# Kernel tuning notes

Hardware: AMD Instinct MI355X
Metric: run time of the kernel (lower is better)

Reference implementation:

```python
import jax, jax.numpy as jnp
import numpy as np

S_NUM, E_NUM, K, B = 50000, 20000, 128, 8192
N = S_NUM + E_NUM
N_EDGES = 1000000
LAYERS = 3


def setup_inputs() -> dict:
    key = jax.random.key(0)
    ks = jax.random.split(key, 16)
    return {
        "stu_emb": jax.random.normal(ks[0], (S_NUM, K), jnp.float32),
        "exer_emb": jax.random.normal(ks[1], (E_NUM, K), jnp.float32),
        "kn_emb": jax.random.normal(ks[2], (K, K), jnp.float32),
        "disc_emb": jax.random.normal(ks[3], (E_NUM, 1), jnp.float32),
        "right_W": jax.random.normal(ks[4], (LAYERS, K, K), jnp.float32) * (1.0 / np.sqrt(K)),
        "wrong_W": jax.random.normal(ks[5], (LAYERS, K, K), jnp.float32) * (1.0 / np.sqrt(K)),
        "right_ci": jax.random.uniform(ks[6], (N, 1), jnp.float32),
        "right_cj": jax.random.uniform(ks[7], (N, 1), jnp.float32),
        "wrong_ci": jax.random.uniform(ks[8], (N, 1), jnp.float32),
        "wrong_cj": jax.random.uniform(ks[9], (N, 1), jnp.float32),
        "right_edges": jax.random.randint(ks[10], (2, N_EDGES), 0, N, jnp.int64),
        "wrong_edges": jax.random.randint(ks[11], (2, N_EDGES), 0, N, jnp.int64),
        "student_id": jax.random.randint(ks[12], (B,), 0, S_NUM, jnp.int64),
        "exercise_id": jax.random.randint(ks[13], (B,), 0, E_NUM, jnp.int64),
    }


def _gcmc_layer(feat, W, cj, ci, src, dst, n_nodes):
    # dense projection + src-side normalizer (dropout is identity in eval)
    h = (feat @ W) * cj                    # [N, K]
    # copy_u/sum message passing: scatter-add messages to destination nodes
    agg = jax.ops.segment_sum(h[src], dst, num_segments=n_nodes)  # [N, K]
    return agg * ci


def _graph_forward(feat, Ws, ci, cj, edges, n_nodes):
    src, dst = edges[0], edges[1]
    for i in range(Ws.shape[0]):
        feat = _gcmc_layer(feat, Ws[i], cj, ci, src, dst, n_nodes)
    return feat


def reference(stu_emb, exer_emb, kn_emb, disc_emb, right_W, wrong_W,
              right_ci, right_cj, wrong_ci, wrong_cj,
              right_edges, wrong_edges, student_id, exercise_id):
    n_students = stu_emb.shape[0]
    n_nodes = stu_emb.shape[0] + exer_emb.shape[0]
    all_weight = jnp.concatenate([stu_emb, exer_emb], axis=0)  # [N, K]
    w1 = _graph_forward(all_weight, right_W, right_ci, right_cj, right_edges, n_nodes)
    w2 = _graph_forward(all_weight, wrong_W, wrong_ci, wrong_cj, wrong_edges, n_nodes)
    stu_forward = w1[:n_students] + w2[:n_students]
    exer_forward = w1[n_students:] + w2[n_students:]
    batch_stu_ts = stu_forward[student_id]      # [B, K]
    batch_exer_ts = exer_forward[exercise_id]   # [B, K]
    disc_ts = disc_emb[exercise_id]             # [B, 1]
    knowledge_ts = kn_emb                       # [K, K]
    return (batch_stu_ts, batch_exer_ts, disc_ts, knowledge_ts)
```

## Files before the change

### kernel.cpp

```cpp
#include <hip/hip_runtime.h>
#include <hip/hip_bf16.h>
#include <stdint.h>

#define S_NUM 50000
#define E_NUM 20000
#define NNODE 70000
#define KDIM 128
#define BATCH 8192
#define NEDGE 1000000

#define NRANGE 128
#define RSZ 547
#define BUCKET_CAP 8448
#define RCAP 16672
#define CHUNK 8192
#define BINCAP 120
#define GR 256
#define CAPC 16384

typedef __attribute__((ext_vector_type(8))) short short8;
typedef __attribute__((ext_vector_type(4))) float f32x4;
typedef __attribute__((ext_vector_type(2))) float f32x2;

__device__ __forceinline__ float bf2f(ushort u) {
    union { uint32_t i; float f; } v; v.i = ((uint32_t)u) << 16; return v.f;
}
__device__ __forceinline__ ushort f2bf(float f) {
    union { uint32_t i; float f; } v; v.f = f;
    uint32_t r = v.i + 0x7fffu + ((v.i >> 16) & 1u);
    return (ushort)(r >> 16);
}
__device__ __forceinline__ f32x2 up2(uint32_t u) {
    union { uint32_t i; float f; } lo, hi;
    lo.i = u << 16; hi.i = u & 0xffff0000u;
    f32x2 r; r.x = lo.f; r.y = hi.f; return r;
}

__global__ void prepW_k(const float* __restrict__ rW, const float* __restrict__ wW,
                        ushort* __restrict__ ws, int* __restrict__ gbcnt,
                        int* __restrict__ flags, int* __restrict__ nsel) {
    int t = blockIdx.x * blockDim.x + threadIdx.x;
    if (blockIdx.x == 0 && threadIdx.x < 256) gbcnt[threadIdx.x] = 0;
    if (t == 0) nsel[0] = 0;
    if (t < NNODE) flags[t] = 0;
    if (t >= 6 * 16384) return;
    int m = t >> 14, idx = t & 16383;
    const float* W = (m < 3) ? rW + m * 16384 : wW + (m - 3) * 16384;
    float x = W[idx];
    int k = idx >> 7, c = idx & 127;
    ushort hb = f2bf(x);
    ushort lb = f2bf(x - bf2f(hb));
    int off = ((c * 256 + 2 * k) ^ ((c & 7) << 4)) >> 1;
    ws[(size_t)m * 32768 + off] = hb;
    ws[(size_t)m * 32768 + 16384 + off] = lb;
}

__global__ __launch_bounds__(256) void bucket_k(const int* __restrict__ redge,
                                                const int* __restrict__ wedge,
                                                int* __restrict__ gbcnt,
                                                uint32_t* __restrict__ bpk) {
    __shared__ uint32_t lpk[NRANGE][BINCAP];
    __shared__ int lcnt[NRANGE];
    __shared__ int gbase[NRANGE];
    const int NB = (NEDGE + CHUNK - 1) / CHUNK;
    int bid = blockIdx.x;
    int graph = bid >= NB;
    int cb = graph ? bid - NB : bid;
    const int* eg = graph ? wedge : redge;
    int e0 = cb * CHUNK;
    int nthis = min(CHUNK, NEDGE - e0);
    for (int i = threadIdx.x; i < NRANGE; i += 256) lcnt[i] = 0;
    __syncthreads();
    for (int i = threadIdx.x; i < nthis; i += 256) {
        int s = eg[e0 + i];
        int d = eg[NEDGE + e0 + i];
        int b = d / RSZ;
        uint32_t p = ((uint32_t)(d - b * RSZ) << 17) | (uint32_t)s;
        int slot = atomicAdd(&lcnt[b], 1);
        if (slot < BINCAP) lpk[b][slot] = p;
        else {
            int gs = atomicAdd(&gbcnt[graph * NRANGE + b], 1);
            if (gs < BUCKET_CAP)
                bpk[(size_t)(graph * NRANGE + b) * BUCKET_CAP + gs] = p;
        }
    }
    __syncthreads();
    for (int b = threadIdx.x; b < NRANGE; b += 256) {
        int c = min(lcnt[b], BINCAP);
        lcnt[b] = c;
        gbase[b] = atomicAdd(&gbcnt[graph * NRANGE + b], c);
    }
    __syncthreads();
    for (int b = 0; b < NRANGE; ++b) {
        int c = lcnt[b];
        size_t base = (size_t)(graph * NRANGE + b) * BUCKET_CAP + gbase[b];
        for (int i = threadIdx.x; i < c; i += 256)
            if (gbase[b] + i < BUCKET_CAP) bpk[base + i] = lpk[b][i];
    }
}

__global__ __launch_bounds__(256) void build_k(const uint32_t* __restrict__ bpk,
                                               const int* __restrict__ gbcnt,
                                               int* __restrict__ rpb,
                                               int* __restrict__ rpe,
                                               int* __restrict__ csr) {
    __shared__ int lcnt[RSZ];
    __shared__ int lexcl[RSZ];
    __shared__ int pexcl[RSZ];
    __shared__ int lcur[RSZ];
    __shared__ int sliceB[BUCKET_CAP];
    __shared__ int wsum[4];
    __shared__ int s_carry;
    int combo = blockIdx.x;
    int graph = combo >> 7, grp = combo & (NRANGE - 1);
    int lo = grp * RSZ;
    int rsize = min(RSZ, NNODE - lo);
    int n = min(gbcnt[combo], BUCKET_CAP);
    const uint32_t* bp = bpk + (size_t)combo * BUCKET_CAP;
    int* rpbg = rpb + graph * NNODE;
    int* rpeg = rpe + graph * NNODE;
    int* og = csr + (size_t)combo * RCAP;
    const int rbase = combo * RCAP;
    int tid = threadIdx.x, lane = tid & 63, wid = tid >> 6;

    for (int i = tid; i < rsize; i += 256) lcnt[i] = 0;
    if (tid == 0) s_carry = 0;
    __syncthreads();
    for (int i = tid; i < n; i += 256)
        atomicAdd(&lcnt[bp[i] >> 17], 1);
    __syncthreads();
    for (int base = 0; base < rsize; base += 256) {
        int i = base + tid;
        int v = (i < rsize) ? lcnt[i] : 0;
        int incl = v;
        #pragma unroll
        for (int off = 1; off < 64; off <<= 1) {
            int t = __shfl_up(incl, off, 64);
            if (lane >= off) incl += t;
        }
        if (lane == 63) wsum[wid] = incl;
        __syncthreads();
        int carry = s_carry;
        if (wid == 0 && lane < 4) {
            int wv = wsum[lane];
            #pragma unroll
            for (int off = 1; off < 4; off <<= 1) {
                int t = __shfl_up(wv, off, 64);
                if (lane >= off) wv += t;
            }
            wsum[lane] = wv;
        }
        __syncthreads();
        int waveoff = (wid == 0) ? 0 : wsum[wid - 1];
        int excl = carry + waveoff + incl - v;
        if (i < rsize) { lexcl[i] = excl; lcur[i] = excl; }
        __syncthreads();
        if (tid == 0) s_carry = carry + wsum[3];
        __syncthreads();
    }
    if (tid == 0) s_carry = 0;
    __syncthreads();
    for (int base = 0; base < rsize; base += 256) {
        int i = base + tid;
        int v = (i < rsize) ? ((lcnt[i] + 15) & ~15) : 0;
        int incl = v;
        #pragma unroll
        for (int off = 1; off < 64; off <<= 1) {
            int t = __shfl_up(incl, off, 64);
            if (lane >= off) incl += t;
        }
        if (lane == 63) wsum[wid] = incl;
        __syncthreads();
        int carry = s_carry;
        if (wid == 0 && lane < 4) {
            int wv = wsum[lane];
            #pragma unroll
            for (int off = 1; off < 4; off <<= 1) {
                int t = __shfl_up(wv, off, 64);
                if (lane >= off) wv += t;
            }
            wsum[lane] = wv;
        }
        __syncthreads();
        int waveoff = (wid == 0) ? 0 : wsum[wid - 1];
        int excl = carry + waveoff + incl - v;
        if (i < rsize) pexcl[i] = excl;
        __syncthreads();
        if (tid == 0) s_carry = carry + wsum[3];
        __syncthreads();
    }
    for (int i = tid; i < rsize; i += 256) {
        int pc = (lcnt[i] + 15) & ~15;
        rpbg[lo + i] = rbase + pexcl[i];
        rpeg[lo + i] = rbase + pexcl[i] + pc;
    }
    for (int i = tid; i < n; i += 256) {
        uint32_t p = bp[i];
        int slot = atomicAdd(&lcur[p >> 17], 1);
        sliceB[slot] = (int)p;
    }
    __syncthreads();
    for (int i = tid; i < n; i += 256) {
        uint32_t p = (uint32_t)sliceB[i];
        int r = p >> 17;
        og[pexcl[r] + (i - lexcl[r])] = (int)(p & 0x1FFFFu);
    }
    for (int r = tid; r < rsize; r += 256) {
        int c = lcnt[r], pc = (c + 15) & ~15, b = pexcl[r];
        for (int j = c; j < pc; ++j) og[b + j] = NNODE;
    }
}

__global__ void mark_k(const int* __restrict__ sid, const int* __restrict__ eid,
                       int* __restrict__ flags) {
    int i = blockIdx.x * blockDim.x + threadIdx.x;
    if (i < BATCH) flags[sid[i]] = 1;
    else if (i < 2 * BATCH) flags[S_NUM + eid[i - BATCH]] = 1;
}

__global__ void compact_k(const int* __restrict__ flags, int* __restrict__ list,
                          int* __restrict__ inv, int* __restrict__ nsel) {
    for (int i = blockIdx.x * blockDim.x + threadIdx.x; i < NNODE;
         i += gridDim.x * blockDim.x) {
        if (flags[i]) {
            int pos = atomicAdd(nsel, 1);
            list[pos] = i;
            inv[i] = pos;
        }
    }
}

__global__ __launch_bounds__(256) void cvt1_k(const float* __restrict__ stu,
                                              const float* __restrict__ exer,
                                              const float* __restrict__ rcj,
                                              const float* __restrict__ wcj,
                                              uint4* __restrict__ featb,
                                              uint4* __restrict__ fcR,
                                              uint4* __restrict__ fcW,
                                              float* __restrict__ cjpR,
                                              float* __restrict__ cjpW) {
    const int main = NNODE * 16;
    const int total = main + 48 + 2 * (NNODE + 1);
    const uint4 z4 = {0, 0, 0, 0};
    for (int i = blockIdx.x * blockDim.x + threadIdx.x; i < total;
         i += gridDim.x * blockDim.x) {
        if (i < main) {
            int node = i >> 4;
            int qq = i & 15;
            const float4* src = (const float4*)((node < S_NUM)
                                  ? stu + (size_t)node * KDIM
                                  : exer + (size_t)(node - S_NUM) * KDIM);
            float4 a = src[qq * 2];
            float4 b = src[qq * 2 + 1];
            uint4 o;
            o.x = (uint32_t)f2bf(a.x) | ((uint32_t)f2bf(a.y) << 16);
            o.y = (uint32_t)f2bf(a.z) | ((uint32_t)f2bf(a.w) << 16);
            o.z = (uint32_t)f2bf(b.x) | ((uint32_t)f2bf(b.y) << 16);
            o.w = (uint32_t)f2bf(b.z) | ((uint32_t)f2bf(b.w) << 16);
            featb[i] = o;
        } else if (i < main + 48) {
            int j = i - main;
            size_t off = (size_t)NNODE * 16 + (j & 15);
            switch (j >> 4) {
                case 0: featb[off] = z4; break;
                case 1: fcR[off] = z4; break;
                default: fcW[off] = z4; break;
            }
        } else {
            int k = i - main - 48;
            if (k <= NNODE)  cjpR[k] = (k < NNODE) ? rcj[k] : 0.f;
            else {
                int m = k - (NNODE + 1);
                cjpW[m] = (m < NNODE) ? wcj[m] : 0.f;
            }
        }
    }
}

template<int USECJ, int COMPACT>
__global__ __launch_bounds__(256) void agg2_k(const uint4* __restrict__ srcR,
                                              const uint4* __restrict__ srcW,
                                              const float* __restrict__ cjR,
                                              const float* __restrict__ cjW,
                                              const int* __restrict__ rpb,
                                              const int* __restrict__ rpe,
                                              const int* __restrict__ csr,
                                              const int* __restrict__ list,
                                              const int* __restrict__ nselp,
                                              uint4* __restrict__ outR,
                                              uint4* __restrict__ outW) {
    int lane = threadIdx.x & 63, wid = threadIdx.x >> 6;
    int grp = lane >> 4, c16 = lane & 15;
    int gi = blockIdx.x * 16 + wid * 4 + grp;
    int graph, n, orow;
    if (COMPACT) {
        int nsel = nselp[0];
        graph = gi >= CAPC;
        int ci = graph ? gi - CAPC : gi;
        if (ci >= nsel) return;
        n = list[ci];
        orow = ci;
    } else {
        if (gi >= 2 * NNODE) return;
        graph = gi >= NNODE;
        n = graph ? gi - NNODE : gi;
        orow = n;
    }
    const uint4* fc = graph ? srcW : srcR;
    const float* cjg = graph ? cjW : cjR;
    int beg = (rpb + graph * NNODE)[n];
    int end = (rpe + graph * NNODE)[n];
    uint4* outp = graph ? outW : outR;

    f32x2 a0 = {0.f, 0.f}, a1 = {0.f, 0.f}, a2 = {0.f, 0.f}, a3 = {0.f, 0.f};
    for (int e = beg; e < end; e += 8) {
        int s0 = csr[e],     s1 = csr[e + 1], s2 = csr[e + 2], s3 = csr[e + 3];
        int s4 = csr[e + 4], s5 = csr[e + 5], s6 = csr[e + 6], s7 = csr[e + 7];
        uint4 u0 = fc[(size_t)s0 * 16 + c16];
        uint4 u1 = fc[(size_t)s1 * 16 + c16];
        uint4 u2 = fc[(size_t)s2 * 16 + c16];
        uint4 u3 = fc[(size_t)s3 * 16 + c16];
        uint4 u4 = fc[(size_t)s4 * 16 + c16];
        uint4 u5 = fc[(size_t)s5 * 16 + c16];
        uint4 u6 = fc[(size_t)s6 * 16 + c16];
        uint4 u7 = fc[(size_t)s7 * 16 + c16];
        if (USECJ) {
            float c0 = cjg[s0], c1 = cjg[s1], c2 = cjg[s2], c3 = cjg[s3];
            float c4 = cjg[s4], c5 = cjg[s5], c6 = cjg[s6], c7 = cjg[s7];
            f32x2 v0 = {c0, c0}, v1 = {c1, c1}, v2 = {c2, c2}, v3 = {c3, c3};
            f32x2 v4 = {c4, c4}, v5 = {c5, c5}, v6 = {c6, c6}, v7 = {c7, c7};
            a0 += v0 * up2(u0.x) + v1 * up2(u1.x) + v2 * up2(u2.x) + v3 * up2(u3.x)
                + v4 * up2(u4.x) + v5 * up2(u5.x) + v6 * up2(u6.x) + v7 * up2(u7.x);
            a1 += v0 * up2(u0.y) + v1 * up2(u1.y) + v2 * up2(u2.y) + v3 * up2(u3.y)
                + v4 * up2(u4.y) + v5 * up2(u5.y) + v6 * up2(u6.y) + v7 * up2(u7.y);
            a2 += v0 * up2(u0.z) + v1 * up2(u1.z) + v2 * up2(u2.z) + v3 * up2(u3.z)
                + v4 * up2(u4.z) + v5 * up2(u5.z) + v6 * up2(u6.z) + v7 * up2(u7.z);
            a3 += v0 * up2(u0.w) + v1 * up2(u1.w) + v2 * up2(u2.w) + v3 * up2(u3.w)
                + v4 * up2(u4.w) + v5 * up2(u5.w) + v6 * up2(u6.w) + v7 * up2(u7.w);
        } else {
            a0 += (up2(u0.x) + up2(u1.x)) + (up2(u2.x) + up2(u3.x))
                + (up2(u4.x) + up2(u5.x)) + (up2(u6.x) + up2(u7.x));
            a1 += (up2(u0.y) + up2(u1.y)) + (up2(u2.y) + up2(u3.y))
                + (up2(u4.y) + up2(u5.y)) + (up2(u6.y) + up2(u7.y));
            a2 += (up2(u0.z) + up2(u1.z)) + (up2(u2.z) + up2(u3.z))
                + (up2(u4.z) + up2(u5.z)) + (up2(u6.z) + up2(u7.z));
            a3 += (up2(u0.w) + up2(u1.w)) + (up2(u2.w) + up2(u3.w))
                + (up2(u4.w) + up2(u5.w)) + (up2(u6.w) + up2(u7.w));
        }
    }
    uint4 o;
    o.x = (uint32_t)f2bf(a0.x) | ((uint32_t)f2bf(a0.y) << 16);
    o.y = (uint32_t)f2bf(a1.x) | ((uint32_t)f2bf(a1.y) << 16);
    o.z = (uint32_t)f2bf(a2.x) | ((uint32_t)f2bf(a2.y) << 16);
    o.w = (uint32_t)f2bf(a3.x) | ((uint32_t)f2bf(a3.y) << 16);
    outp[(size_t)orow * 16 + c16] = o;
}

template<int COMPACT>
__global__ __launch_bounds__(256) void gemm2_k(const ushort* __restrict__ AR,
                                               const ushort* __restrict__ AW,
                                               const ushort* __restrict__ wsR,
                                               const ushort* __restrict__ wsW,
                                               const float* __restrict__ rci,
                                               const float* __restrict__ rcj,
                                               const float* __restrict__ wci,
                                               const float* __restrict__ wcj,
                                               const int* __restrict__ list,
                                               const int* __restrict__ nselp,
                                               ushort* __restrict__ outR,
                                               ushort* __restrict__ outW,
                                               int mode) {
    const int halfBlocks = COMPACT ? (CAPC / GR) : ((NNODE + GR - 1) / GR);
    int graph = blockIdx.x >= halfBlocks;
    int bb = graph ? blockIdx.x - halfBlocks : blockIdx.x;
    int nrows = COMPACT ? nselp[0] : NNODE;
    const ushort* A = graph ? AW : AR;
    const ushort* wsm = graph ? wsW : wsR;
    const float* ci = graph ? wci : rci;
    const float* cj = graph ? wcj : rcj;
    ushort* outB = graph ? outW : outR;

    __shared__ ushort wt[32768];
    {
        const uint4* g = (const uint4*)wsm;
        uint4* l = (uint4*)wt;
        for (int i = threadIdx.x; i < 4096; i += 256) l[i] = g[i];
    }
    __syncthreads();

    int wid = threadIdx.x >> 6, lane = threadIdx.x & 63;
    int q = lane >> 4, l16 = lane & 15;
    int rbase = bb * GR + wid * 64;
    if (rbase >= nrows) return;

    short8 z8 = {0, 0, 0, 0, 0, 0, 0, 0};
    short8 afr[4][4];
    #pragma unroll
    for (int t = 0; t < 4; ++t) {
        int row = rbase + t * 16 + l16;
        bool rok = row < nrows;
        const short8* ar = (const short8*)(A + (size_t)row * KDIM);
        #pragma unroll
        for (int kb = 0; kb < 4; ++kb)
            afr[t][kb] = rok ? ar[kb * 4 + q] : z8;
    }
    float scal[4][4];
    #pragma unroll
    for (int t = 0; t < 4; ++t)
        #pragma unroll
        for (int b = 0; b < 4; ++b) {
            int r = rbase + t * 16 + q * 4 + b;
            bool ok = r < nrows;
            int node = COMPACT ? (ok ? list[r] : 0) : r;
            scal[t][b] = ok ? (mode ? ci[node] * cj[node] : ci[node]) : 0.f;
        }

    #pragma unroll
    for (int cb = 0; cb < 8; ++cb) {
        int c = cb * 16 + l16;
        short8 bHi[4], bLo[4];
        #pragma unroll
        for (int kb = 0; kb < 4; ++kb) {
            int byte = (c * 256 + 2 * (kb * 32 + q * 8)) ^ ((c & 7) << 4);
            bHi[kb] = *(const short8*)((const char*)wt + byte);
            bLo[kb] = *(const short8*)((const char*)wt + 32768 + byte);
        }
        #pragma unroll
        for (int t = 0; t < 4; ++t) {
            f32x4 acc = {0.f, 0.f, 0.f, 0.f};
            #pragma unroll
            for (int kb = 0; kb < 4; ++kb) {
                acc = __builtin_amdgcn_mfma_f32_16x16x32_bf16(afr[t][kb], bHi[kb], acc, 0, 0, 0);
                acc = __builtin_amdgcn_mfma_f32_16x16x32_bf16(afr[t][kb], bLo[kb], acc, 0, 0, 0);
            }
            #pragma unroll
            for (int b = 0; b < 4; ++b) {
                int r = rbase + t * 16 + q * 4 + b;
                if (r < nrows)
                    outB[(size_t)r * KDIM + c] = f2bf(acc[b] * scal[t][b]);
            }
        }
    }
}

__global__ void out_k(const ushort* __restrict__ w1c, const ushort* __restrict__ w2c,
                      const int* __restrict__ inv,
                      const float* __restrict__ disc, const float* __restrict__ kn,
                      const int* __restrict__ sid, const int* __restrict__ eid,
                      float* __restrict__ out) {
    const int total = 2 * BATCH * KDIM + BATCH + KDIM * KDIM;
    for (int i = blockIdx.x * blockDim.x + threadIdx.x; i < total;
         i += gridDim.x * blockDim.x) {
        if (i < BATCH * KDIM) {
            int b = i >> 7, c = i & 127;
            size_t r = (size_t)inv[sid[b]];
            out[i] = bf2f(w1c[r * KDIM + c]) + bf2f(w2c[r * KDIM + c]);
        } else if (i < 2 * BATCH * KDIM) {
            int j = i - BATCH * KDIM;
            int b = j >> 7, c = j & 127;
            size_t r = (size_t)inv[S_NUM + eid[b]];
            out[i] = bf2f(w1c[r * KDIM + c]) + bf2f(w2c[r * KDIM + c]);
        } else if (i < 2 * BATCH * KDIM + BATCH) {
            out[i] = disc[eid[i - 2 * BATCH * KDIM]];
        } else {
            out[i] = kn[i - (2 * BATCH * KDIM + BATCH)];
        }
    }
}

static inline size_t align_up(size_t x) { return (x + 255) & ~(size_t)255; }

extern "C" void kernel_launch(void* const* d_in, const int* in_sizes, int n_in,
                              void* d_out, int out_size, void* d_ws, size_t ws_size,
                              hipStream_t stream) {
    const float* stu  = (const float*)d_in[0];
    const float* exer = (const float*)d_in[1];
    const float* kn   = (const float*)d_in[2];
    const float* disc = (const float*)d_in[3];
    const float* rW   = (const float*)d_in[4];
    const float* wW   = (const float*)d_in[5];
    const float* rci  = (const float*)d_in[6];
    const float* rcj  = (const float*)d_in[7];
    const float* wci  = (const float*)d_in[8];
    const float* wcj  = (const float*)d_in[9];
    const int* redge   = (const int*)d_in[10];
    const int* wedge   = (const int*)d_in[11];
    const int* sid     = (const int*)d_in[12];
    const int* eid     = (const int*)d_in[13];
    float* out         = (float*)d_out;

    char* p = (char*)d_ws;
    const size_t fB16 = align_up((size_t)(NNODE + 1) * KDIM * 2);
    ushort* featb = (ushort*)p; p += fB16;
    ushort* fcR = (ushort*)p; p += fB16;
    ushort* fcW = (ushort*)p; p += fB16;
    ushort* pR  = (ushort*)p; p += fB16;
    ushort* pW  = (ushort*)p; p += fB16;
    ushort* ws  = (ushort*)p; p += align_up((size_t)6 * 32768 * 2);
    int* gbcnt = (int*)p; p += align_up((size_t)256 * 4);
    int* rpb = (int*)p; p += align_up((size_t)2 * NNODE * 4);
    int* rpe = (int*)p; p += align_up((size_t)2 * NNODE * 4);
    int* csr = (int*)p; p += align_up((size_t)256 * RCAP * 4);
    float* cjpR = (float*)p; p += align_up((size_t)(NNODE + 1) * 4);
    float* cjpW = (float*)p; p += align_up((size_t)(NNODE + 1) * 4);
    int* flags = (int*)p; p += align_up((size_t)NNODE * 4);
    int* list  = (int*)p; p += align_up((size_t)CAPC * 4);
    int* inv   = (int*)p; p += align_up((size_t)NNODE * 4);
    int* nsel  = (int*)p; p += align_up((size_t)16 * 4);
    uint32_t* bpk = (uint32_t*)pR;
    ushort* w1c = featb;
    ushort* w2c = featb + (size_t)CAPC * KDIM;

    const int aggFull = (2 * NNODE + 15) / 16;
    const int aggComp = 2 * CAPC / 16;
    const int gemmFull = 2 * ((NNODE + GR - 1) / GR);
    const int gemmComp = 2 * (CAPC / GR);
    const int NB = (NEDGE + CHUNK - 1) / CHUNK;

    prepW_k<<<(6 * 16384 + 255) / 256, 256, 0, stream>>>(rW, wW, ws, gbcnt, flags, nsel);
    bucket_k<<<2 * NB, 256, 0, stream>>>(redge, wedge, gbcnt, bpk);
    build_k<<<256, 256, 0, stream>>>(bpk, gbcnt, rpb, rpe, csr);
    mark_k<<<(2 * BATCH + 255) / 256, 256, 0, stream>>>(sid, eid, flags);
    compact_k<<<(NNODE + 255) / 256, 256, 0, stream>>>(flags, list, inv, nsel);
    cvt1_k<<<2048, 256, 0, stream>>>(stu, exer, rcj, wcj, (uint4*)featb,
                                     (uint4*)fcR, (uint4*)fcW, cjpR, cjpW);

    agg2_k<1, 0><<<aggFull, 256, 0, stream>>>((const uint4*)featb, (const uint4*)featb,
                                              cjpR, cjpW, rpb, rpe, csr, nullptr, nullptr,
                                              (uint4*)pR, (uint4*)pW);
    gemm2_k<0><<<gemmFull, 256, 0, stream>>>(pR, pW, ws + 0 * 32768, ws + 3 * 32768,
                                             rci, rcj, wci, wcj, nullptr, nullptr,
                                             fcR, fcW, 1);
    agg2_k<0, 0><<<aggFull, 256, 0, stream>>>((const uint4*)fcR, (const uint4*)fcW,
                                              nullptr, nullptr, rpb, rpe, csr,
                                              nullptr, nullptr, (uint4*)pR, (uint4*)pW);
    gemm2_k<0><<<gemmFull, 256, 0, stream>>>(pR, pW, ws + 1 * 32768, ws + 4 * 32768,
                                             rci, rcj, wci, wcj, nullptr, nullptr,
                                             fcR, fcW, 1);
    agg2_k<0, 1><<<aggComp, 256, 0, stream>>>((const uint4*)fcR, (const uint4*)fcW,
                                              nullptr, nullptr, rpb, rpe, csr,
                                              list, nsel, (uint4*)pR, (uint4*)pW);
    gemm2_k<1><<<gemmComp, 256, 0, stream>>>(pR, pW, ws + 2 * 32768, ws + 5 * 32768,
                                             rci, rcj, wci, wcj, list, nsel,
                                             w1c, w2c, 0);

    out_k<<<2048, 256, 0, stream>>>(w1c, w2c, inv, disc, kn, sid, eid, out);
}
```

Measured before the change: 349.7 us.

## Split node features into four 32-column planes for cache-friendly gather aggregation

Stores bf16 node features as four column planes of 32 elements each, so every plane is about 4.5MB and fits in cache. The aggregation kernel now gives each block one plane and one graph, with 4 lanes per node reading 64 contiguous bytes, instead of 16 lanes reading a full 256-byte row. The GEMM input and output indexing and the conversion kernel are updated to match, and CSR indices are loaded as int4. The intent is to raise L2/MALL hit rates on random gathers, at the cost of reading the CSR index lists four times and doing narrower per-node work.

```diff
diff --git a/kernel.cpp b/kernel.cpp
--- a/kernel.cpp
+++ b/kernel.cpp
@@ -17,6 +17,7 @@
 #define BINCAP 120
 #define GR 256
 #define CAPC 16384
+#define NT 4
 
 typedef __attribute__((ext_vector_type(8))) short short8;
 typedef __attribute__((ext_vector_type(4))) float f32x4;
@@ -35,6 +36,12 @@
     lo.i = u << 16; hi.i = u & 0xffff0000u;
     f32x2 r; r.x = lo.f; r.y = hi.f; return r;
 }
+__device__ __forceinline__ uint32_t pk2(f32x2 a) {
+    return (uint32_t)f2bf(a.x) | ((uint32_t)f2bf(a.y) << 16);
+}
+
+#define PLANE_E ((size_t)(NNODE + 1) * 32)
+#define PLANE_U4 ((size_t)(NNODE + 1) * 4)
 
 __global__ void prepW_k(const float* __restrict__ rW, const float* __restrict__ wW,
                         ushort* __restrict__ ws, int* __restrict__ gbcnt,
@@ -257,15 +264,15 @@
             o.y = (uint32_t)f2bf(a.z) | ((uint32_t)f2bf(a.w) << 16);
             o.z = (uint32_t)f2bf(b.x) | ((uint32_t)f2bf(b.y) << 16);
             o.w = (uint32_t)f2bf(b.z) | ((uint32_t)f2bf(b.w) << 16);
-            featb[i] = o;
+            featb[(size_t)(qq >> 2) * PLANE_U4 + (size_t)node * 4 + (qq & 3)] = o;
         } else if (i < main + 48) {
             int j = i - main;
-            size_t off = (size_t)NNODE * 16 + (j & 15);
-            switch (j >> 4) {
-                case 0: featb[off] = z4; break;
-                case 1: fcR[off] = z4; break;
-                default: fcW[off] = z4; break;
-            }
+            int arr = j >> 4;
+            int jj = j & 15;
+            size_t off = (size_t)(jj >> 2) * PLANE_U4 + (size_t)NNODE * 4 + (jj & 3);
+            if (arr == 0)      featb[off] = z4;
+            else if (arr == 1) fcR[off] = z4;
+            else               fcW[off] = z4;
         } else {
             int k = i - main - 48;
             if (k <= NNODE)  cjpR[k] = (k < NNODE) ? rcj[k] : 0.f;
@@ -289,44 +296,40 @@
                                               const int* __restrict__ nselp,
                                               uint4* __restrict__ outR,
                                               uint4* __restrict__ outW) {
-    int lane = threadIdx.x & 63, wid = threadIdx.x >> 6;
-    int grp = lane >> 4, c16 = lane & 15;
-    int gi = blockIdx.x * 16 + wid * 4 + grp;
-    int graph, n, orow;
+    int combo = blockIdx.x & 7;
+    int tile = combo & 3, graph = combo >> 2;
+    int ci = (blockIdx.x >> 3) * 64 + (threadIdx.x >> 2);
+    int l4 = threadIdx.x & 3;
+    int n, orow;
     if (COMPACT) {
-        int nsel = nselp[0];
-        graph = gi >= CAPC;
-        int ci = graph ? gi - CAPC : gi;
-        if (ci >= nsel) return;
-        n = list[ci];
-        orow = ci;
+        if (ci >= nselp[0]) return;
+        n = list[ci]; orow = ci;
     } else {
-        if (gi >= 2 * NNODE) return;
-        graph = gi >= NNODE;
-        n = graph ? gi - NNODE : gi;
-        orow = n;
-    }
-    const uint4* fc = graph ? srcW : srcR;
+        if (ci >= NNODE) return;
+        n = ci; orow = ci;
+    }
+    const uint4* fc = (graph ? srcW : srcR) + (size_t)tile * PLANE_U4;
     const float* cjg = graph ? cjW : cjR;
     int beg = (rpb + graph * NNODE)[n];
     int end = (rpe + graph * NNODE)[n];
-    uint4* outp = graph ? outW : outR;
-
+    uint4* outp = (graph ? outW : outR) + (size_t)tile * PLANE_U4;
+
+    const int4* csr4 = (const int4*)csr;
     f32x2 a0 = {0.f, 0.f}, a1 = {0.f, 0.f}, a2 = {0.f, 0.f}, a3 = {0.f, 0.f};
     for (int e = beg; e < end; e += 8) {
-        int s0 = csr[e],     s1 = csr[e + 1], s2 = csr[e + 2], s3 = csr[e + 3];
-        int s4 = csr[e + 4], s5 = csr[e + 5], s6 = csr[e + 6], s7 = csr[e + 7];
-        uint4 u0 = fc[(size_t)s0 * 16 + c16];
-        uint4 u1 = fc[(size_t)s1 * 16 + c16];
-        uint4 u2 = fc[(size_t)s2 * 16 + c16];
-        uint4 u3 = fc[(size_t)s3 * 16 + c16];
-        uint4 u4 = fc[(size_t)s4 * 16 + c16];
-        uint4 u5 = fc[(size_t)s5 * 16 + c16];
-        uint4 u6 = fc[(size_t)s6 * 16 + c16];
-        uint4 u7 = fc[(size_t)s7 * 16 + c16];
+        int4 sa = csr4[e >> 2];
+        int4 sb = csr4[(e >> 2) + 1];
+        uint4 u0 = fc[(size_t)sa.x * 4 + l4];
+        uint4 u1 = fc[(size_t)sa.y * 4 + l4];
+        uint4 u2 = fc[(size_t)sa.z * 4 + l4];
+        uint4 u3 = fc[(size_t)sa.w * 4 + l4];
+        uint4 u4 = fc[(size_t)sb.x * 4 + l4];
+        uint4 u5 = fc[(size_t)sb.y * 4 + l4];
+        uint4 u6 = fc[(size_t)sb.z * 4 + l4];
+        uint4 u7 = fc[(size_t)sb.w * 4 + l4];
         if (USECJ) {
-            float c0 = cjg[s0], c1 = cjg[s1], c2 = cjg[s2], c3 = cjg[s3];
-            float c4 = cjg[s4], c5 = cjg[s5], c6 = cjg[s6], c7 = cjg[s7];
+            float c0 = cjg[sa.x], c1 = cjg[sa.y], c2 = cjg[sa.z], c3 = cjg[sa.w];
+            float c4 = cjg[sb.x], c5 = cjg[sb.y], c6 = cjg[sb.z], c7 = cjg[sb.w];
             f32x2 v0 = {c0, c0}, v1 = {c1, c1}, v2 = {c2, c2}, v3 = {c3, c3};
             f32x2 v4 = {c4, c4}, v5 = {c5, c5}, v6 = {c6, c6}, v7 = {c7, c7};
             a0 += v0 * up2(u0.x) + v1 * up2(u1.x) + v2 * up2(u2.x) + v3 * up2(u3.x)
@@ -349,11 +352,8 @@
         }
     }
     uint4 o;
-    o.x = (uint32_t)f2bf(a0.x) | ((uint32_t)f2bf(a0.y) << 16);
-    o.y = (uint32_t)f2bf(a1.x) | ((uint32_t)f2bf(a1.y) << 16);
-    o.z = (uint32_t)f2bf(a2.x) | ((uint32_t)f2bf(a2.y) << 16);
-    o.w = (uint32_t)f2bf(a3.x) | ((uint32_t)f2bf(a3.y) << 16);
-    outp[(size_t)orow * 16 + c16] = o;
+    o.x = pk2(a0); o.y = pk2(a1); o.z = pk2(a2); o.w = pk2(a3);
+    outp[(size_t)orow * 4 + l4] = o;
 }
 
 template<int COMPACT>
@@ -399,10 +399,11 @@
     for (int t = 0; t < 4; ++t) {
         int row = rbase + t * 16 + l16;
         bool rok = row < nrows;
-        const short8* ar = (const short8*)(A + (size_t)row * KDIM);
         #pragma unroll
         for (int kb = 0; kb < 4; ++kb)
-            afr[t][kb] = rok ? ar[kb * 4 + q] : z8;
+            afr[t][kb] = rok ? *(const short8*)(A + (size_t)kb * PLANE_E
+                                                + (size_t)row * 32 + q * 8)
+                             : z8;
     }
     float scal[4][4];
     #pragma unroll
@@ -436,8 +437,11 @@
             #pragma unroll
             for (int b = 0; b < 4; ++b) {
                 int r = rbase + t * 16 + q * 4 + b;
-                if (r < nrows)
-                    outB[(size_t)r * KDIM + c] = f2bf(acc[b] * scal[t][b]);
+                if (r < nrows) {
+                    ushort v = f2bf(acc[b] * scal[t][b]);
+                    if (COMPACT) outB[(size_t)r * KDIM + c] = v;
+                    else outB[(size_t)(c >> 5) * PLANE_E + (size_t)r * 32 + (c & 31)] = v;
+                }
             }
         }
     }
@@ -490,7 +494,7 @@
     float* out         = (float*)d_out;
 
     char* p = (char*)d_ws;
-    const size_t fB16 = align_up((size_t)(NNODE + 1) * KDIM * 2);
+    const size_t fB16 = align_up((size_t)NT * PLANE_E * 2);
     ushort* featb = (ushort*)p; p += fB16;
     ushort* fcR = (ushort*)p; p += fB16;
     ushort* fcW = (ushort*)p; p += fB16;
@@ -511,8 +515,8 @@
     ushort* w1c = featb;
     ushort* w2c = featb + (size_t)CAPC * KDIM;
 
-    const int aggFull = (2 * NNODE + 15) / 16;
-    const int aggComp = 2 * CAPC / 16;
+    const int aggFull = 8 * ((NNODE + 63) / 64);
+    const int aggComp = 8 * (CAPC / 64);
     const int gemmFull = 2 * ((NNODE + GR - 1) / GR);
     const int gemmComp = 2 * (CAPC / GR);
     const int NB = (NEDGE + CHUNK - 1) / CHUNK;
```

After: 374.2 us. +7.0%, slower.

## Fold three layer weight matrices into one product and defer GEMM to selected rows

Applied to the files above, without the earlier changes.

Since each layer is linear and the per-node scalings commute with the right multiplication by W, the three per-layer GEMMs are replaced by one precomputed product W1·W2·W3 per graph. It is applied only to the compacted rows needed for the output. Aggregation passes now carry per-source weights (cj, then ci*cj) instead of running intermediate full-size GEMMs. This removes two full-node GEMM passes at the cost of a small weight-product prelude. Intermediate features are kept in unprojected bf16 form, which changes rounding behaviour.

```diff
diff --git a/kernel.cpp b/kernel.cpp
--- a/kernel.cpp
+++ b/kernel.cpp
@@ -35,24 +35,66 @@
     lo.i = u << 16; hi.i = u & 0xffff0000u;
     f32x2 r; r.x = lo.f; r.y = hi.f; return r;
 }
-
-__global__ void prepW_k(const float* __restrict__ rW, const float* __restrict__ wW,
-                        ushort* __restrict__ ws, int* __restrict__ gbcnt,
-                        int* __restrict__ flags, int* __restrict__ nsel) {
-    int t = blockIdx.x * blockDim.x + threadIdx.x;
-    if (blockIdx.x == 0 && threadIdx.x < 256) gbcnt[threadIdx.x] = 0;
-    if (t == 0) nsel[0] = 0;
-    if (t < NNODE) flags[t] = 0;
-    if (t >= 6 * 16384) return;
-    int m = t >> 14, idx = t & 16383;
-    const float* W = (m < 3) ? rW + m * 16384 : wW + (m - 3) * 16384;
-    float x = W[idx];
-    int k = idx >> 7, c = idx & 127;
-    ushort hb = f2bf(x);
-    ushort lb = f2bf(x - bf2f(hb));
-    int off = ((c * 256 + 2 * k) ^ ((c & 7) << 4)) >> 1;
-    ws[(size_t)m * 32768 + off] = hb;
-    ws[(size_t)m * 32768 + 16384 + off] = lb;
+__device__ __forceinline__ uint32_t pk2(f32x2 a) {
+    return (uint32_t)f2bf(a.x) | ((uint32_t)f2bf(a.y) << 16);
+}
+
+__global__ __launch_bounds__(256) void prep0_k(const float* __restrict__ rW,
+                                               const float* __restrict__ wW,
+                                               float* __restrict__ Tprod,
+                                               int* __restrict__ gbcnt,
+                                               int* __restrict__ flags,
+                                               int* __restrict__ nsel) {
+    int b = blockIdx.x;
+    if (b < 8) {
+        int g = b >> 2, cq = b & 3;
+        const float* W1 = g ? wW : rW;
+        const float* W2 = (g ? wW : rW) + 16384;
+        __shared__ float w2q[128][32];
+        for (int i = threadIdx.x; i < 4096; i += 256)
+            w2q[i >> 5][i & 31] = W2[(i >> 5) * 128 + cq * 32 + (i & 31)];
+        __syncthreads();
+        for (int o = threadIdx.x; o < 4096; o += 256) {
+            int r = o >> 5, c = o & 31;
+            float acc = 0.f;
+            #pragma unroll 4
+            for (int k = 0; k < 128; ++k)
+                acc = fmaf(W1[r * 128 + k], w2q[k][c], acc);
+            Tprod[(size_t)g * 16384 + r * 128 + cq * 32 + c] = acc;
+        }
+    } else {
+        int t = (b - 8) * 256 + threadIdx.x;
+        if (t < NNODE) flags[t] = 0;
+        if (t < 256) gbcnt[t] = 0;
+        if (t == 0) nsel[0] = 0;
+    }
+}
+
+__global__ __launch_bounds__(256) void wprod2_k(const float* __restrict__ Tprod,
+                                                const float* __restrict__ rW,
+                                                const float* __restrict__ wW,
+                                                ushort* __restrict__ ws) {
+    int g = blockIdx.x >> 2, cq = blockIdx.x & 3;
+    const float* T = Tprod + (size_t)g * 16384;
+    const float* W3 = (g ? wW : rW) + 2 * 16384;
+    __shared__ float w3q[128][32];
+    for (int i = threadIdx.x; i < 4096; i += 256)
+        w3q[i >> 5][i & 31] = W3[(i >> 5) * 128 + cq * 32 + (i & 31)];
+    __syncthreads();
+    ushort* wsg = ws + (size_t)g * 32768;
+    for (int o = threadIdx.x; o < 4096; o += 256) {
+        int r = o >> 5, cc = o & 31;
+        int c = cq * 32 + cc;
+        float acc = 0.f;
+        #pragma unroll 4
+        for (int k = 0; k < 128; ++k)
+            acc = fmaf(T[r * 128 + k], w3q[k][cc], acc);
+        ushort hb = f2bf(acc);
+        ushort lb = f2bf(acc - bf2f(hb));
+        int off = ((c * 256 + 2 * r) ^ ((c & 7) << 4)) >> 1;
+        wsg[off] = hb;
+        wsg[16384 + off] = lb;
+    }
 }
 
 __global__ __launch_bounds__(256) void bucket_k(const int* __restrict__ redge,
@@ -230,17 +272,22 @@
     }
 }
 
-__global__ __launch_bounds__(256) void cvt1_k(const float* __restrict__ stu,
-                                              const float* __restrict__ exer,
-                                              const float* __restrict__ rcj,
-                                              const float* __restrict__ wcj,
-                                              uint4* __restrict__ featb,
-                                              uint4* __restrict__ fcR,
-                                              uint4* __restrict__ fcW,
-                                              float* __restrict__ cjpR,
-                                              float* __restrict__ cjpW) {
+__global__ __launch_bounds__(256) void cvt_k(const float* __restrict__ stu,
+                                             const float* __restrict__ exer,
+                                             const float* __restrict__ rci,
+                                             const float* __restrict__ rcj,
+                                             const float* __restrict__ wci,
+                                             const float* __restrict__ wcj,
+                                             uint4* __restrict__ featb,
+                                             uint4* __restrict__ pR,
+                                             uint4* __restrict__ pW,
+                                             uint4* __restrict__ qW,
+                                             float* __restrict__ cjpR,
+                                             float* __restrict__ cjpW,
+                                             float* __restrict__ ccR,
+                                             float* __restrict__ ccW) {
     const int main = NNODE * 16;
-    const int total = main + 48 + 2 * (NNODE + 1);
+    const int total = main + 64 + (NNODE + 1);
     const uint4 z4 = {0, 0, 0, 0};
     for (int i = blockIdx.x * blockDim.x + threadIdx.x; i < total;
          i += gridDim.x * blockDim.x) {
@@ -258,37 +305,38 @@
             o.z = (uint32_t)f2bf(b.x) | ((uint32_t)f2bf(b.y) << 16);
             o.w = (uint32_t)f2bf(b.z) | ((uint32_t)f2bf(b.w) << 16);
             featb[i] = o;
-        } else if (i < main + 48) {
+        } else if (i < main + 64) {
             int j = i - main;
             size_t off = (size_t)NNODE * 16 + (j & 15);
             switch (j >> 4) {
                 case 0: featb[off] = z4; break;
-                case 1: fcR[off] = z4; break;
-                default: fcW[off] = z4; break;
+                case 1: pR[off] = z4; break;
+                case 2: pW[off] = z4; break;
+                default: qW[off] = z4; break;
             }
         } else {
-            int k = i - main - 48;
-            if (k <= NNODE)  cjpR[k] = (k < NNODE) ? rcj[k] : 0.f;
-            else {
-                int m = k - (NNODE + 1);
-                cjpW[m] = (m < NNODE) ? wcj[m] : 0.f;
-            }
-        }
-    }
-}
-
-template<int USECJ, int COMPACT>
-__global__ __launch_bounds__(256) void agg2_k(const uint4* __restrict__ srcR,
-                                              const uint4* __restrict__ srcW,
-                                              const float* __restrict__ cjR,
-                                              const float* __restrict__ cjW,
-                                              const int* __restrict__ rpb,
-                                              const int* __restrict__ rpe,
-                                              const int* __restrict__ csr,
-                                              const int* __restrict__ list,
-                                              const int* __restrict__ nselp,
-                                              uint4* __restrict__ outR,
-                                              uint4* __restrict__ outW) {
+            int k = i - main - 64;
+            bool in = k < NNODE;
+            cjpR[k] = in ? rcj[k] : 0.f;
+            cjpW[k] = in ? wcj[k] : 0.f;
+            ccR[k] = in ? rci[k] * rcj[k] : 0.f;
+            ccW[k] = in ? wci[k] * wcj[k] : 0.f;
+        }
+    }
+}
+
+template<int COMPACT>
+__global__ __launch_bounds__(256) void agg_k(const uint4* __restrict__ srcR,
+                                             const uint4* __restrict__ srcW,
+                                             const float* __restrict__ wR,
+                                             const float* __restrict__ wWt,
+                                             const int* __restrict__ rpb,
+                                             const int* __restrict__ rpe,
+                                             const int* __restrict__ csr,
+                                             const int* __restrict__ list,
+                                             const int* __restrict__ nselp,
+                                             uint4* __restrict__ outR,
+                                             uint4* __restrict__ outW) {
     int lane = threadIdx.x & 63, wid = threadIdx.x >> 6;
     int grp = lane >> 4, c16 = lane & 15;
     int gi = blockIdx.x * 16 + wid * 4 + grp;
@@ -307,7 +355,7 @@
         orow = n;
     }
     const uint4* fc = graph ? srcW : srcR;
-    const float* cjg = graph ? cjW : cjR;
+    const float* wg = graph ? wWt : wR;
     int beg = (rpb + graph * NNODE)[n];
     int end = (rpe + graph * NNODE)[n];
     uint4* outp = graph ? outW : outR;
@@ -324,61 +372,41 @@
         uint4 u5 = fc[(size_t)s5 * 16 + c16];
         uint4 u6 = fc[(size_t)s6 * 16 + c16];
         uint4 u7 = fc[(size_t)s7 * 16 + c16];
-        if (USECJ) {
-            float c0 = cjg[s0], c1 = cjg[s1], c2 = cjg[s2], c3 = cjg[s3];
-            float c4 = cjg[s4], c5 = cjg[s5], c6 = cjg[s6], c7 = cjg[s7];
-            f32x2 v0 = {c0, c0}, v1 = {c1, c1}, v2 = {c2, c2}, v3 = {c3, c3};
-            f32x2 v4 = {c4, c4}, v5 = {c5, c5}, v6 = {c6, c6}, v7 = {c7, c7};
-            a0 += v0 * up2(u0.x) + v1 * up2(u1.x) + v2 * up2(u2.x) + v3 * up2(u3.x)
-                + v4 * up2(u4.x) + v5 * up2(u5.x) + v6 * up2(u6.x) + v7 * up2(u7.x);
-            a1 += v0 * up2(u0.y) + v1 * up2(u1.y) + v2 * up2(u2.y) + v3 * up2(u3.y)
-                + v4 * up2(u4.y) + v5 * up2(u5.y) + v6 * up2(u6.y) + v7 * up2(u7.y);
-            a2 += v0 * up2(u0.z) + v1 * up2(u1.z) + v2 * up2(u2.z) + v3 * up2(u3.z)
-                + v4 * up2(u4.z) + v5 * up2(u5.z) + v6 * up2(u6.z) + v7 * up2(u7.z);
-            a3 += v0 * up2(u0.w) + v1 * up2(u1.w) + v2 * up2(u2.w) + v3 * up2(u3.w)
-                + v4 * up2(u4.w) + v5 * up2(u5.w) + v6 * up2(u6.w) + v7 * up2(u7.w);
-        } else {
-            a0 += (up2(u0.x) + up2(u1.x)) + (up2(u2.x) + up2(u3.x))
-                + (up2(u4.x) + up2(u5.x)) + (up2(u6.x) + up2(u7.x));
-            a1 += (up2(u0.y) + up2(u1.y)) + (up2(u2.y) + up2(u3.y))
-                + (up2(u4.y) + up2(u5.y)) + (up2(u6.y) + up2(u7.y));
-            a2 += (up2(u0.z) + up2(u1.z)) + (up2(u2.z) + up2(u3.z))
-                + (up2(u4.z) + up2(u5.z)) + (up2(u6.z) + up2(u7.z));
-            a3 += (up2(u0.w) + up2(u1.w)) + (up2(u2.w) + up2(u3.w))
-                + (up2(u4.w) + up2(u5.w)) + (up2(u6.w) + up2(u7.w));
-        }
+        float c0 = wg[s0], c1 = wg[s1], c2 = wg[s2], c3 = wg[s3];
+        float c4 = wg[s4], c5 = wg[s5], c6 = wg[s6], c7 = wg[s7];
+        f32x2 v0 = {c0, c0}, v1 = {c1, c1}, v2 = {c2, c2}, v3 = {c3, c3};
+        f32x2 v4 = {c4, c4}, v5 = {c5, c5}, v6 = {c6, c6}, v7 = {c7, c7};
+        a0 += v0 * up2(u0.x) + v1 * up2(u1.x) + v2 * up2(u2.x) + v3 * up2(u3.x)
+            + v4 * up2(u4.x) + v5 * up2(u5.x) + v6 * up2(u6.x) + v7 * up2(u7.x);
+        a1 += v0 * up2(u0.y) + v1 * up2(u1.y) + v2 * up2(u2.y) + v3 * up2(u3.y)
+            + v4 * up2(u4.y) + v5 * up2(u5.y) + v6 * up2(u6.y) + v7 * up2(u7.y);
+        a2 += v0 * up2(u0.z) + v1 * up2(u1.z) + v2 * up2(u2.z) + v3 * up2(u3.z)
+            + v4 * up2(u4.z) + v5 * up2(u5.z) + v6 * up2(u6.z) + v7 * up2(u7.z);
+        a3 += v0 * up2(u0.w) + v1 * up2(u1.w) + v2 * up2(u2.w) + v3 * up2(u3.w)
+            + v4 * up2(u4.w) + v5 * up2(u5.w) + v6 * up2(u6.w) + v7 * up2(u7.w);
     }
     uint4 o;
-    o.x = (uint32_t)f2bf(a0.x) | ((uint32_t)f2bf(a0.y) << 16);
-    o.y = (uint32_t)f2bf(a1.x) | ((uint32_t)f2bf(a1.y) << 16);
-    o.z = (uint32_t)f2bf(a2.x) | ((uint32_t)f2bf(a2.y) << 16);
-    o.w = (uint32_t)f2bf(a3.x) | ((uint32_t)f2bf(a3.y) << 16);
+    o.x = pk2(a0); o.y = pk2(a1); o.z = pk2(a2); o.w = pk2(a3);
     outp[(size_t)orow * 16 + c16] = o;
 }
 
-template<int COMPACT>
-__global__ __launch_bounds__(256) void gemm2_k(const ushort* __restrict__ AR,
+__global__ __launch_bounds__(256) void gemmc_k(const ushort* __restrict__ AR,
                                                const ushort* __restrict__ AW,
-                                               const ushort* __restrict__ wsR,
-                                               const ushort* __restrict__ wsW,
+                                               const ushort* __restrict__ ws,
                                                const float* __restrict__ rci,
-                                               const float* __restrict__ rcj,
                                                const float* __restrict__ wci,
-                                               const float* __restrict__ wcj,
                                                const int* __restrict__ list,
                                                const int* __restrict__ nselp,
-                                               ushort* __restrict__ outR,
-                                               ushort* __restrict__ outW,
-                                               int mode) {
-    const int halfBlocks = COMPACT ? (CAPC / GR) : ((NNODE + GR - 1) / GR);
+                                               ushort* __restrict__ w1c,
+                                               ushort* __restrict__ w2c) {
+    const int halfBlocks = CAPC / GR;
     int graph = blockIdx.x >= halfBlocks;
     int bb = graph ? blockIdx.x - halfBlocks : blockIdx.x;
-    int nrows = COMPACT ? nselp[0] : NNODE;
+    int nrows = nselp[0];
     const ushort* A = graph ? AW : AR;
-    const ushort* wsm = graph ? wsW : wsR;
+    const ushort* wsm = ws + (size_t)graph * 32768;
     const float* ci = graph ? wci : rci;
-    const float* cj = graph ? wcj : rcj;
-    ushort* outB = graph ? outW : outR;
+    ushort* outB = graph ? w2c : w1c;
 
     __shared__ ushort wt[32768];
     {
@@ -411,8 +439,8 @@
         for (int b = 0; b < 4; ++b) {
             int r = rbase + t * 16 + q * 4 + b;
             bool ok = r < nrows;
-            int node = COMPACT ? (ok ? list[r] : 0) : r;
-            scal[t][b] = ok ? (mode ? ci[node] * cj[node] : ci[node]) : 0.f;
+            int node = ok ? list[r] : 0;
+            scal[t][b] = ok ? ci[node] : 0.f;
         }
 
     #pragma unroll
@@ -492,57 +520,53 @@
     char* p = (char*)d_ws;
     const size_t fB16 = align_up((size_t)(NNODE + 1) * KDIM * 2);
     ushort* featb = (ushort*)p; p += fB16;
-    ushort* fcR = (ushort*)p; p += fB16;
-    ushort* fcW = (ushort*)p; p += fB16;
     ushort* pR  = (ushort*)p; p += fB16;
     ushort* pW  = (ushort*)p; p += fB16;
-    ushort* ws  = (ushort*)p; p += align_up((size_t)6 * 32768 * 2);
+    ushort* qW  = (ushort*)p; p += fB16;
+    ushort* ws  = (ushort*)p; p += align_up((size_t)2 * 32768 * 2);
+    float* Tprod = (float*)p; p += align_up((size_t)2 * 16384 * 4);
     int* gbcnt = (int*)p; p += align_up((size_t)256 * 4);
     int* rpb = (int*)p; p += align_up((size_t)2 * NNODE * 4);
     int* rpe = (int*)p; p += align_up((size_t)2 * NNODE * 4);
     int* csr = (int*)p; p += align_up((size_t)256 * RCAP * 4);
     float* cjpR = (float*)p; p += align_up((size_t)(NNODE + 1) * 4);
     float* cjpW = (float*)p; p += align_up((size_t)(NNODE + 1) * 4);
+    float* ccR  = (float*)p; p += align_up((size_t)(NNODE + 1) * 4);
+    float* ccW  = (float*)p; p += align_up((size_t)(NNODE + 1) * 4);
     int* flags = (int*)p; p += align_up((size_t)NNODE * 4);
     int* list  = (int*)p; p += align_up((size_t)CAPC * 4);
     int* inv   = (int*)p; p += align_up((size_t)NNODE * 4);
     int* nsel  = (int*)p; p += align_up((size_t)16 * 4);
     uint32_t* bpk = (uint32_t*)pR;
+    ushort* qR = featb;
     ushort* w1c = featb;
     ushort* w2c = featb + (size_t)CAPC * KDIM;
 
     const int aggFull = (2 * NNODE + 15) / 16;
     const int aggComp = 2 * CAPC / 16;
-    const int gemmFull = 2 * ((NNODE + GR - 1) / GR);
     const int gemmComp = 2 * (CAPC / GR);
     const int NB = (NEDGE + CHUNK - 1) / CHUNK;
 
-    prepW_k<<<(6 * 16384 + 255) / 256, 256, 0, stream>>>(rW, wW, ws, gbcnt, flags, nsel);
+    prep0_k<<<8 + (NNODE + 255) / 256, 256, 0, stream>>>(rW, wW, Tprod, gbcnt, flags, nsel);
+    wprod2_k<<<8, 256, 0, stream>>>(Tprod, rW, wW, ws);
     bucket_k<<<2 * NB, 256, 0, stream>>>(redge, wedge, gbcnt, bpk);
     build_k<<<256, 256, 0, stream>>>(bpk, gbcnt, rpb, rpe, csr);
     mark_k<<<(2 * BATCH + 255) / 256, 256, 0, stream>>>(sid, eid, flags);
     compact_k<<<(NNODE + 255) / 256, 256, 0, stream>>>(flags, list, inv, nsel);
-    cvt1_k<<<2048, 256, 0, stream>>>(stu, exer, rcj, wcj, (uint4*)featb,
-                                     (uint4*)fcR, (uint4*)fcW, cjpR, cjpW);
-
-    agg2_k<1, 0><<<aggFull, 256, 0, stream>>>((const uint4*)featb, (const uint4*)featb,
-                                              cjpR, cjpW, rpb, rpe, csr, nullptr, nullptr,
-                                              (uint4*)pR, (uint4*)pW);
-    gemm2_k<0><<<gemmFull, 256, 0, stream>>>(pR, pW, ws + 0 * 32768, ws + 3 * 32768,
-                                             rci, rcj, wci, wcj, nullptr, nullptr,
-                                             fcR, fcW, 1);
-    agg2_k<0, 0><<<aggFull, 256, 0, stream>>>((const uint4*)fcR, (const uint4*)fcW,
-                                              nullptr, nullptr, rpb, rpe, csr,
-                                              nullptr, nullptr, (uint4*)pR, (uint4*)pW);
-    gemm2_k<0><<<gemmFull, 256, 0, stream>>>(pR, pW, ws + 1 * 32768, ws + 4 * 32768,
-                                             rci, rcj, wci, wcj, nullptr, nullptr,
-                                             fcR, fcW, 1);
-    agg2_k<0, 1><<<aggComp, 256, 0, stream>>>((const uint4*)fcR, (const uint4*)fcW,
-                                              nullptr, nullptr, rpb, rpe, csr,
-                                              list, nsel, (uint4*)pR, (uint4*)pW);
-    gemm2_k<1><<<gemmComp, 256, 0, stream>>>(pR, pW, ws + 2 * 32768, ws + 5 * 32768,
-                                             rci, rcj, wci, wcj, list, nsel,
-                                             w1c, w2c, 0);
+    cvt_k<<<2048, 256, 0, stream>>>(stu, exer, rci, rcj, wci, wcj, (uint4*)featb,
+                                    (uint4*)pR, (uint4*)pW, (uint4*)qW,
+                                    cjpR, cjpW, ccR, ccW);
+
+    agg_k<0><<<aggFull, 256, 0, stream>>>((const uint4*)featb, (const uint4*)featb,
+                                          cjpR, cjpW, rpb, rpe, csr, nullptr, nullptr,
+                                          (uint4*)pR, (uint4*)pW);
+    agg_k<0><<<aggFull, 256, 0, stream>>>((const uint4*)pR, (const uint4*)pW,
+                                          ccR, ccW, rpb, rpe, csr, nullptr, nullptr,
+                                          (uint4*)qR, (uint4*)qW);
+    agg_k<1><<<aggComp, 256, 0, stream>>>((const uint4*)qR, (const uint4*)qW,
+                                          ccR, ccW, rpb, rpe, csr, list, nsel,
+                                          (uint4*)pR, (uint4*)pW);
+    gemmc_k<<<gemmComp, 256, 0, stream>>>(pR, pW, ws, rci, wci, list, nsel, w1c, w2c);
 
     out_k<<<2048, 256, 0, stream>>>(w1c, w2c, inv, disc, kn, sid, eid, out);
 }
```

Result: slower. 375.1 us (+7.2%).
